# Performance work log

Measured on AMD Instinct MI355X. Metric: run time of the kernel, lower is better.

The kernel has to match this reference:

```python
import jax, jax.numpy as jnp
import numpy as np

BS, SEQ_LEN, DIM = 8, 16, 512
DIM_QK, DIM_V = 512, 512
MAX_BS, MAX_SEQ = 8, 8192
START_POS = 4096
KV_LEN = START_POS + SEQ_LEN


def setup_inputs() -> dict:
    key = jax.random.key(0)
    ks = jax.random.split(key, 8)
    w_scale = 0.02
    return {
        "x": jax.random.normal(ks[0], (BS, SEQ_LEN, DIM), dtype=jnp.float32),
        "start_pos": START_POS,
        "mask": jnp.zeros((SEQ_LEN, KV_LEN), dtype=jnp.float32),
        "Wq": jax.random.normal(ks[1], (DIM_QK, DIM), dtype=jnp.float32) * w_scale,
        "Wk": jax.random.normal(ks[2], (DIM_QK, DIM), dtype=jnp.float32) * w_scale,
        "Wv": jax.random.normal(ks[3], (DIM_V, DIM), dtype=jnp.float32) * w_scale,
        "Wo": jax.random.normal(ks[4], (DIM, DIM_V), dtype=jnp.float32) * w_scale,
        "cache_k": jax.random.normal(ks[5], (MAX_BS, MAX_SEQ, DIM_QK), dtype=jnp.float32) * 0.1,
        "cache_v": jax.random.normal(ks[6], (MAX_BS, MAX_SEQ, DIM_V), dtype=jnp.float32) * 0.1,
    }


def reference(x, start_pos, mask, Wq, Wk, Wv, Wo, cache_k, cache_v):
    bs, seq_len, _ = x.shape
    dim_qk = Wq.shape[0]
    scale = (dim_qk // 2) ** (-0.5)  # note: source uses dim_qk//2, not dim_qk

    # projections (torch Linear: y = x @ W.T, W is [out, in])
    q = jnp.einsum('bsd,ed->bse', x, Wq)
    k = jnp.einsum('bsd,ed->bse', x, Wk)
    v = jnp.einsum('bsd,ed->bse', x, Wv)

    # KV-cache append + read (start_pos is static)
    cache_k = jax.lax.dynamic_update_slice(cache_k, k, (0, start_pos, 0))
    cache_v = jax.lax.dynamic_update_slice(cache_v, v, (0, start_pos, 0))
    k_full = cache_k[:bs, :start_pos + seq_len]  # [bs, kv_len, dim_qk]
    v_full = cache_v[:bs, :start_pos + seq_len]  # [bs, kv_len, dim_v]

    dist = jnp.einsum('bqd,bkd->bqk', q, k_full) * scale  # [bs, q, kv]
    weight = jax.lax.stop_gradient(dist)
    dist = dist + mask  # additive mask, broadcast over batch
    probs = jax.nn.softmax(dist, axis=-1)
    atten = jnp.einsum('bqk,bkv->bqv', probs, v_full)
    out = jnp.einsum('bqv,ev->bqe', atten, Wo)
    return (out, weight)
```

## Files before the change

### kernel.cpp

```cpp
#include <hip/hip_runtime.h>

#define BSZ 8
#define SEQ 16
#define DIMN 512
#define SP 4096
#define KVL 4112

#define SCALE 0.0625f

#define PPART 0
#define QBUF  786432
#define KNEW  851968
#define VNEW  917504
#define PROBS 983040
#define APART 1509376
#define ATTEN 5769216
#define OPART 5834752

__global__ __launch_bounds__(64) void proj_partial(
    const float* __restrict__ X, const float* __restrict__ W0,
    const float* __restrict__ W1, const float* __restrict__ W2,
    float* __restrict__ outbase)
{
  __shared__ float xs[SEQ][128];
  int b = blockIdx.x >> 2, et = blockIdx.x & 3;
  int dt = blockIdx.y, m = blockIdx.z;
  const float* W = (m == 0) ? W0 : (m == 1) ? W1 : W2;
  float* outp = outbase + (size_t)m * (4 * 65536) + (size_t)dt * 65536;
  int t = threadIdx.x;

  const float4* xsrc = (const float4*)(X + (size_t)(b * SEQ) * DIMN + dt * 128);
  for (int i = t; i < SEQ * 32; i += 64) {
    int row = i >> 5, j = i & 31;
    *(float4*)&xs[row][j * 4] = xsrc[row * 128 + j];
  }
  __syncthreads();

  int r0 = (t >> 5) * 8;
  int e = et * 128 + (t & 31) * 4;
  float acc[8][4];
#pragma unroll
  for (int r = 0; r < 8; ++r)
#pragma unroll
    for (int i = 0; i < 4; ++i) acc[r][i] = 0.f;

  const float* wbase = W + dt * 128;
  for (int d4 = 0; d4 < 32; ++d4) {
    float4 w[4];
#pragma unroll
    for (int i = 0; i < 4; ++i)
      w[i] = *(const float4*)(wbase + (size_t)(e + i) * DIMN + d4 * 4);
#pragma unroll
    for (int r = 0; r < 8; ++r) {
      float4 xv = *(const float4*)&xs[r0 + r][d4 * 4];
#pragma unroll
      for (int i = 0; i < 4; ++i)
        acc[r][i] += xv.x * w[i].x + xv.y * w[i].y + xv.z * w[i].z + xv.w * w[i].w;
    }
  }
#pragma unroll
  for (int r = 0; r < 8; ++r) {
    float4 o = make_float4(acc[r][0], acc[r][1], acc[r][2], acc[r][3]);
    *(float4*)(outp + (size_t)(b * SEQ + r0 + r) * DIMN + e) = o;
  }
}

__global__ __launch_bounds__(256) void reduce_dt(
    const float* __restrict__ src, float* __restrict__ dst, int nm)
{
  int idx = blockIdx.x * 256 + threadIdx.x;
  if (idx >= nm * 65536) return;
  int m = idx >> 16, j = idx & 65535;
  const float* s = src + (size_t)m * (4 * 65536);
  dst[idx] = s[j] + s[65536 + j] + s[2 * 65536 + j] + s[3 * 65536 + j];
}

__global__ __launch_bounds__(256) void scores_kernel(
    const float* __restrict__ qbuf, const float* __restrict__ cache_k,
    const float* __restrict__ knew, float* __restrict__ weight)
{
  int b = blockIdx.x;
  int p0 = blockIdx.y * 64;
  int len = KVL - p0; if (len > 64) len = 64;
  int t = threadIdx.x, lane = t & 63, w = t >> 6;

  float4 qa[SEQ], qb[SEQ];
  const float* qbase = qbuf + (size_t)b * SEQ * DIMN + lane * 8;
#pragma unroll
  for (int s = 0; s < SEQ; ++s) {
    qa[s] = *(const float4*)(qbase + s * DIMN);
    qb[s] = *(const float4*)(qbase + s * DIMN + 4);
  }

  bool b1 = (lane & 1), b2 = (lane & 2), b4 = (lane & 4), b8 = (lane & 8);
  int niter = (len - w + 3) >> 2;
#pragma unroll 2
  for (int i = 0; i < niter; ++i) {
    int p = p0 + w + 4 * i;
    const float* krow = (p < SP)
        ? (cache_k + ((size_t)b * 8192 + p) * DIMN)
        : (knew + (size_t)(b * SEQ + (p - SP)) * DIMN);
    float4 ka = *(const float4*)(krow + lane * 8);
    float4 kb = *(const float4*)(krow + lane * 8 + 4);

    float acc[SEQ];
#pragma unroll
    for (int s = 0; s < SEQ; ++s) {
      acc[s] = qa[s].x * ka.x + qa[s].y * ka.y + qa[s].z * ka.z + qa[s].w * ka.w
             + qb[s].x * kb.x + qb[s].y * kb.y + qb[s].z * kb.z + qb[s].w * kb.w;
    }
    float r8[8];
#pragma unroll
    for (int u = 0; u < 8; ++u) {
      float keep = b1 ? acc[u + 8] : acc[u];
      float send = b1 ? acc[u] : acc[u + 8];
      r8[u] = keep + __shfl_xor(send, 1);
    }
    float r4[4];
#pragma unroll
    for (int u = 0; u < 4; ++u) {
      float keep = b2 ? r8[u + 4] : r8[u];
      float send = b2 ? r8[u] : r8[u + 4];
      r4[u] = keep + __shfl_xor(send, 2);
    }
    float r2[2];
#pragma unroll
    for (int u = 0; u < 2; ++u) {
      float keep = b4 ? r4[u + 2] : r4[u];
      float send = b4 ? r4[u] : r4[u + 2];
      r2[u] = keep + __shfl_xor(send, 4);
    }
    float keep = b8 ? r2[1] : r2[0];
    float send = b8 ? r2[0] : r2[1];
    float r1 = keep + __shfl_xor(send, 8);
    r1 += __shfl_xor(r1, 16);
    r1 += __shfl_xor(r1, 32);

    if (lane < 16) {
      int s = ((lane & 1) << 3) | ((lane & 2) << 1) | ((lane & 4) >> 1) | ((lane & 8) >> 3);
      weight[(size_t)(b * SEQ + s) * KVL + p] = r1 * SCALE;
    }
  }
}

__global__ __launch_bounds__(256) void softmax_kernel(
    const float* __restrict__ weight, const float* __restrict__ mask,
    float* __restrict__ probs)
{
  int row = blockIdx.x;
  int s = row & 15;
  int t = threadIdx.x, lane = t & 63, w = t >> 6;
  const float* src = weight + (size_t)row * KVL;
  const float* msk = mask + (size_t)s * KVL;

  float vals[17];
  float mx = -1e30f;
#pragma unroll
  for (int i = 0; i < 17; ++i) {
    int p = t + i * 256;
    if (p < KVL) { vals[i] = src[p] + msk[p]; mx = fmaxf(mx, vals[i]); }
    else vals[i] = -1e30f;
  }
  for (int off = 32; off >= 1; off >>= 1) mx = fmaxf(mx, __shfl_xor(mx, off));
  __shared__ float redm[4], reds[4];
  if (lane == 0) redm[w] = mx;
  __syncthreads();
  mx = fmaxf(fmaxf(redm[0], redm[1]), fmaxf(redm[2], redm[3]));

  float sum = 0.f;
#pragma unroll
  for (int i = 0; i < 17; ++i) {
    int p = t + i * 256;
    if (p < KVL) { vals[i] = __expf(vals[i] - mx); sum += vals[i]; }
  }
  for (int off = 32; off >= 1; off >>= 1) sum += __shfl_xor(sum, off);
  if (lane == 0) reds[w] = sum;
  __syncthreads();
  sum = reds[0] + reds[1] + reds[2] + reds[3];
  float inv = 1.0f / sum;

  float* dst = probs + (size_t)row * KVL;
#pragma unroll
  for (int i = 0; i < 17; ++i) {
    int p = t + i * 256;
    if (p < KVL) dst[p] = vals[i] * inv;
  }
}

__global__ __launch_bounds__(256) void attnv_kernel(
    const float* __restrict__ probs, const float* __restrict__ cache_v,
    const float* __restrict__ vnew, float* __restrict__ apart)
{
  __shared__ float pl[SEQ][64];
  int b = blockIdx.x, c = blockIdx.y;
  int p0 = c * 64;
  int len = KVL - p0; if (len > 64) len = 64;
  int t = threadIdx.x;

  for (int i = t; i < SEQ * 64; i += 256) {
    int q = i >> 6, j = i & 63;
    pl[q][j] = (j < len) ? probs[(size_t)(b * SEQ + q) * KVL + p0 + j] : 0.f;
  }
  __syncthreads();

  float acc0[SEQ], acc1[SEQ];
#pragma unroll
  for (int q = 0; q < SEQ; ++q) { acc0[q] = 0.f; acc1[q] = 0.f; }

  int nj4 = len >> 2;
  for (int j4 = 0; j4 < nj4; ++j4) {
    float4 pv[SEQ];
#pragma unroll
    for (int q = 0; q < SEQ; ++q) pv[q] = *(const float4*)&pl[q][j4 * 4];
#pragma unroll
    for (int jj = 0; jj < 4; ++jj) {
      int p = p0 + j4 * 4 + jj;
      const float* vrow = (p < SP)
          ? (cache_v + ((size_t)b * 8192 + p) * DIMN)
          : (vnew + (size_t)(b * SEQ + (p - SP)) * DIMN);
      float va = vrow[t], vb = vrow[t + 256];
#pragma unroll
      for (int q = 0; q < SEQ; ++q) {
        float pj = (jj == 0) ? pv[q].x : (jj == 1) ? pv[q].y : (jj == 2) ? pv[q].z : pv[q].w;
        acc0[q] += pj * va;
        acc1[q] += pj * vb;
      }
    }
  }
  float* outp = apart + (size_t)c * 65536 + (size_t)b * SEQ * DIMN;
#pragma unroll
  for (int q = 0; q < SEQ; ++q) {
    outp[q * DIMN + t] = acc0[q];
    outp[q * DIMN + t + 256] = acc1[q];
  }
}

__global__ __launch_bounds__(256) void reduce_att(
    const float* __restrict__ apart, float* __restrict__ atten)
{
  int idx = blockIdx.x * 256 + threadIdx.x;
  float s = 0.f;
  for (int c = 0; c < 65; ++c) s += apart[(size_t)c * 65536 + idx];
  atten[idx] = s;
}

extern "C" void kernel_launch(void* const* d_in, const int* in_sizes, int n_in,
                              void* d_out, int out_size, void* d_ws, size_t ws_size,
                              hipStream_t stream) {
  const float* x       = (const float*)d_in[0];
  const float* mask    = (const float*)d_in[2];
  const float* Wq      = (const float*)d_in[3];
  const float* Wk      = (const float*)d_in[4];
  const float* Wv      = (const float*)d_in[5];
  const float* Wo      = (const float*)d_in[6];
  const float* cache_k = (const float*)d_in[7];
  const float* cache_v = (const float*)d_in[8];
  float* out    = (float*)d_out;
  float* weight = out + 65536;
  float* ws     = (float*)d_ws;

  proj_partial<<<dim3(32, 4, 3), 64, 0, stream>>>(x, Wq, Wk, Wv, ws + PPART);
  reduce_dt<<<dim3(768), 256, 0, stream>>>(ws + PPART, ws + QBUF, 3);
  scores_kernel<<<dim3(8, 65), 256, 0, stream>>>(ws + QBUF, cache_k, ws + KNEW, weight);
  softmax_kernel<<<dim3(128), 256, 0, stream>>>(weight, mask, ws + PROBS);
  attnv_kernel<<<dim3(8, 65), 256, 0, stream>>>(ws + PROBS, cache_v, ws + VNEW, ws + APART);
  reduce_att<<<dim3(256), 256, 0, stream>>>(ws + APART, ws + ATTEN);
  proj_partial<<<dim3(32, 4, 1), 64, 0, stream>>>(ws + ATTEN, Wo, Wo, Wo, ws + OPART);
  reduce_dt<<<dim3(256), 256, 0, stream>>>(ws + OPART, out, 1);
}
```

Baseline: 323.2 us.

## Replace split-K projection and reduce with wave-reduction dot-product projection kernel

The tiled split-K projection kernel and its separate reduce kernels are replaced by a proj_dot kernel. Each wave loads all 16 rows of x into registers and computes full-length dot products against weight rows, reducing them with a shuffle tree shared with the scores kernel. This drops two launches and the partial-sum workspace round trip for both the QKV and output projections. The trade-off is that weight rows are now re-read once per batch, eight times in total, with only 8 rows per wave, and the shuffle reduction adds work.

Result: faster. 310.0 us (-4.1%).

```diff
diff --git a/kernel.cpp b/kernel.cpp
--- a/kernel.cpp
+++ b/kernel.cpp
@@ -8,71 +8,85 @@
 
 #define SCALE 0.0625f
 
-#define PPART 0
-#define QBUF  786432
-#define KNEW  851968
-#define VNEW  917504
-#define PROBS 983040
-#define APART 1509376
-#define ATTEN 5769216
-#define OPART 5834752
-
-__global__ __launch_bounds__(64) void proj_partial(
-    const float* __restrict__ X, const float* __restrict__ W0,
-    const float* __restrict__ W1, const float* __restrict__ W2,
-    float* __restrict__ outbase)
-{
-  __shared__ float xs[SEQ][128];
-  int b = blockIdx.x >> 2, et = blockIdx.x & 3;
-  int dt = blockIdx.y, m = blockIdx.z;
-  const float* W = (m == 0) ? W0 : (m == 1) ? W1 : W2;
-  float* outp = outbase + (size_t)m * (4 * 65536) + (size_t)dt * 65536;
-  int t = threadIdx.x;
-
-  const float4* xsrc = (const float4*)(X + (size_t)(b * SEQ) * DIMN + dt * 128);
-  for (int i = t; i < SEQ * 32; i += 64) {
-    int row = i >> 5, j = i & 31;
-    *(float4*)&xs[row][j * 4] = xsrc[row * 128 + j];
-  }
-  __syncthreads();
-
-  int r0 = (t >> 5) * 8;
-  int e = et * 128 + (t & 31) * 4;
-  float acc[8][4];
-#pragma unroll
-  for (int r = 0; r < 8; ++r)
-#pragma unroll
-    for (int i = 0; i < 4; ++i) acc[r][i] = 0.f;
-
-  const float* wbase = W + dt * 128;
-  for (int d4 = 0; d4 < 32; ++d4) {
-    float4 w[4];
-#pragma unroll
-    for (int i = 0; i < 4; ++i)
-      w[i] = *(const float4*)(wbase + (size_t)(e + i) * DIMN + d4 * 4);
-#pragma unroll
-    for (int r = 0; r < 8; ++r) {
-      float4 xv = *(const float4*)&xs[r0 + r][d4 * 4];
-#pragma unroll
-      for (int i = 0; i < 4; ++i)
-        acc[r][i] += xv.x * w[i].x + xv.y * w[i].y + xv.z * w[i].z + xv.w * w[i].w;
-    }
-  }
-#pragma unroll
-  for (int r = 0; r < 8; ++r) {
-    float4 o = make_float4(acc[r][0], acc[r][1], acc[r][2], acc[r][3]);
-    *(float4*)(outp + (size_t)(b * SEQ + r0 + r) * DIMN + e) = o;
-  }
-}
-
-__global__ __launch_bounds__(256) void reduce_dt(
-    const float* __restrict__ src, float* __restrict__ dst, int nm)
-{
-  int idx = blockIdx.x * 256 + threadIdx.x;
-  if (idx >= nm * 65536) return;
-  int m = idx >> 16, j = idx & 65535;
-  const float* s = src + (size_t)m * (4 * 65536);
-  dst[idx] = s[j] + s[65536 + j] + s[2 * 65536 + j] + s[3 * 65536 + j];
+#define QBUF  0
+#define KNEW  65536
+#define VNEW  131072
+#define PROBS 196608
+#define APART 722944
+#define ATTEN 4982784
+
+__device__ __forceinline__ float tree16(const float* acc, bool b1, bool b2, bool b4, bool b8)
+{
+  float r8[8];
+#pragma unroll
+  for (int u = 0; u < 8; ++u) {
+    float keep = b1 ? acc[u + 8] : acc[u];
+    float send = b1 ? acc[u] : acc[u + 8];
+    r8[u] = keep + __shfl_xor(send, 1);
+  }
+  float r4[4];
+#pragma unroll
+  for (int u = 0; u < 4; ++u) {
+    float keep = b2 ? r8[u + 4] : r8[u];
+    float send = b2 ? r8[u] : r8[u + 4];
+    r4[u] = keep + __shfl_xor(send, 2);
+  }
+  float r2[2];
+#pragma unroll
+  for (int u = 0; u < 2; ++u) {
+    float keep = b4 ? r4[u + 2] : r4[u];
+    float send = b4 ? r4[u] : r4[u + 2];
+    r2[u] = keep + __shfl_xor(send, 4);
+  }
+  float keep = b8 ? r2[1] : r2[0];
+  float send = b8 ? r2[0] : r2[1];
+  float r1 = keep + __shfl_xor(send, 8);
+  r1 += __shfl_xor(r1, 16);
+  r1 += __shfl_xor(r1, 32);
+  return r1;
+}
+
+__global__ __launch_bounds__(256) void proj_dot(
+    const float* __restrict__ X,
+    const float* __restrict__ W0, const float* __restrict__ W1,
+    const float* __restrict__ W2,
+    float* __restrict__ D0, float* __restrict__ D1, float* __restrict__ D2)
+{
+  int b = blockIdx.x;
+  int e0 = blockIdx.y * 32;
+  int t = threadIdx.x, lane = t & 63, w = t >> 6;
+
+  float4 xa[SEQ], xb[SEQ];
+  const float* xbase = X + (size_t)b * SEQ * DIMN + lane * 8;
+#pragma unroll
+  for (int s = 0; s < SEQ; ++s) {
+    xa[s] = *(const float4*)(xbase + s * DIMN);
+    xb[s] = *(const float4*)(xbase + s * DIMN + 4);
+  }
+
+  bool b1 = (lane & 1), b2 = (lane & 2), b4 = (lane & 4), b8 = (lane & 8);
+#pragma unroll 2
+  for (int i = 0; i < 8; ++i) {
+    int e = e0 + w + 4 * i;
+    int m = e >> 9, col = e & 511;
+    const float* W = (m == 0) ? W0 : (m == 1) ? W1 : W2;
+    const float* wrow = W + (size_t)col * DIMN + lane * 8;
+    float4 ka = *(const float4*)(wrow);
+    float4 kb = *(const float4*)(wrow + 4);
+
+    float acc[SEQ];
+#pragma unroll
+    for (int s = 0; s < SEQ; ++s) {
+      acc[s] = xa[s].x * ka.x + xa[s].y * ka.y + xa[s].z * ka.z + xa[s].w * ka.w
+             + xb[s].x * kb.x + xb[s].y * kb.y + xb[s].z * kb.z + xb[s].w * kb.w;
+    }
+    float r1 = tree16(acc, b1, b2, b4, b8);
+    if (lane < 16) {
+      int s = ((lane & 1) << 3) | ((lane & 2) << 1) | ((lane & 4) >> 1) | ((lane & 8) >> 3);
+      float* D = (m == 0) ? D0 : (m == 1) ? D1 : D2;
+      D[(size_t)(b * SEQ + s) * DIMN + col] = r1;
+    }
+  }
 }
 
 __global__ __launch_bounds__(256) void scores_kernel(
@@ -109,33 +123,7 @@
       acc[s] = qa[s].x * ka.x + qa[s].y * ka.y + qa[s].z * ka.z + qa[s].w * ka.w
              + qb[s].x * kb.x + qb[s].y * kb.y + qb[s].z * kb.z + qb[s].w * kb.w;
     }
-    float r8[8];
-#pragma unroll
-    for (int u = 0; u < 8; ++u) {
-      float keep = b1 ? acc[u + 8] : acc[u];
-      float send = b1 ? acc[u] : acc[u + 8];
-      r8[u] = keep + __shfl_xor(send, 1);
-    }
-    float r4[4];
-#pragma unroll
-    for (int u = 0; u < 4; ++u) {
-      float keep = b2 ? r8[u + 4] : r8[u];
-      float send = b2 ? r8[u] : r8[u + 4];
-      r4[u] = keep + __shfl_xor(send, 2);
-    }
-    float r2[2];
-#pragma unroll
-    for (int u = 0; u < 2; ++u) {
-      float keep = b4 ? r4[u + 2] : r4[u];
-      float send = b4 ? r4[u] : r4[u + 2];
-      r2[u] = keep + __shfl_xor(send, 4);
-    }
-    float keep = b8 ? r2[1] : r2[0];
-    float send = b8 ? r2[0] : r2[1];
-    float r1 = keep + __shfl_xor(send, 8);
-    r1 += __shfl_xor(r1, 16);
-    r1 += __shfl_xor(r1, 32);
-
+    float r1 = tree16(acc, b1, b2, b4, b8);
     if (lane < 16) {
       int s = ((lane & 1) << 3) | ((lane & 2) << 1) | ((lane & 4) >> 1) | ((lane & 8) >> 3);
       weight[(size_t)(b * SEQ + s) * KVL + p] = r1 * SCALE;
@@ -259,12 +247,12 @@
   float* weight = out + 65536;
   float* ws     = (float*)d_ws;
 
-  proj_partial<<<dim3(32, 4, 3), 64, 0, stream>>>(x, Wq, Wk, Wv, ws + PPART);
-  reduce_dt<<<dim3(768), 256, 0, stream>>>(ws + PPART, ws + QBUF, 3);
+  proj_dot<<<dim3(8, 48), 256, 0, stream>>>(
+      x, Wq, Wk, Wv, ws + QBUF, ws + KNEW, ws + VNEW);
   scores_kernel<<<dim3(8, 65), 256, 0, stream>>>(ws + QBUF, cache_k, ws + KNEW, weight);
   softmax_kernel<<<dim3(128), 256, 0, stream>>>(weight, mask, ws + PROBS);
   attnv_kernel<<<dim3(8, 65), 256, 0, stream>>>(ws + PROBS, cache_v, ws + VNEW, ws + APART);
   reduce_att<<<dim3(256), 256, 0, stream>>>(ws + APART, ws + ATTEN);
-  proj_partial<<<dim3(32, 4, 1), 64, 0, stream>>>(ws + ATTEN, Wo, Wo, Wo, ws + OPART);
-  reduce_dt<<<dim3(256), 256, 0, stream>>>(ws + OPART, out, 1);
-}
+  proj_dot<<<dim3(8, 16), 256, 0, stream>>>(
+      ws + ATTEN, Wo, Wo, Wo, out, out, out);
+}
```
